# Kernel optimization log

Measured on AMD Instinct MI355X. Metric: run time of the kernel, lower is better.

## Reference

```python
import jax, jax.numpy as jnp
import numpy as np

B, H, S, D = 2, 16, 2048, 64

def setup_inputs() -> dict:
    key = jax.random.key(0)
    kq, kk, kv = jax.random.split(key, 3)
    return {
        "query": jax.random.normal(kq, (B, H, S, D), dtype=jnp.float32),
        "key": jax.random.normal(kk, (B, H, S, D), dtype=jnp.float32),
        "value": jax.random.normal(kv, (B, H, S, D), dtype=jnp.float32),
        "mask": 1,
    }

def reference(query, key, value, mask):
    d_k = jnp.asarray(query.shape[-1], dtype=query.dtype)
    # scores: [B, H, S, S] = Q K^T / sqrt(d_k)
    scores = jnp.einsum('bhqd,bhkd->bhqk', query, key) / jnp.sqrt(d_k)
    if mask:
        Sq, Sk = scores.shape[-2], scores.shape[-1]
        causal = jnp.tril(jnp.ones((Sq, Sk), dtype=bool))
        scores = jnp.where(causal, scores, -jnp.inf)
    attention = jax.nn.softmax(scores, axis=-1)
    out = jnp.einsum('bhqk,bhkd->bhqd', attention, value)
    return out, attention
```

## Files before the change

### kernel.cpp

```cpp
#include <hip/hip_runtime.h>


#define B_ 2
#define H_ 16
#define S_ 2048
#define D_ 64
#define QB 8
#define NT 256

typedef unsigned short u16;
typedef unsigned int   u32;
typedef float f32x4 __attribute__((ext_vector_type(4)));

__device__ __forceinline__ float bf2f(u16 h) {
    union { u32 u; float f; } x; x.u = ((u32)h) << 16; return x.f;
}
__device__ __forceinline__ float wred_max(float v) {
    #pragma unroll
    for (int o = 32; o > 0; o >>= 1) v = fmaxf(v, __shfl_xor(v, o, 64));
    return v;
}
__device__ __forceinline__ float wred_sum(float v) {
    #pragma unroll
    for (int o = 32; o > 0; o >>= 1) v += __shfl_xor(v, o, 64);
    return v;
}

__global__ __launch_bounds__(NT)
void attn_tile8_kernel(const void* __restrict__ Qv, const void* __restrict__ Kv,
                       const void* __restrict__ Vv, const int* __restrict__ maskp,
                       float* __restrict__ out, float* __restrict__ att)
{
    const int tid = threadIdx.x;

    const int bid0 = blockIdx.x;
    const int bid  = (bid0 & 7) * 1024 + (bid0 >> 3);

    const int bh = bid >> 8;
    const int q0 = (bid & 255) << 3;
    const int causal = maskp[0];
    const int kmaxB = causal ? (q0 + QB - 1) : (S_ - 1);

    __shared__ float sS[QB * S_];
    __shared__ float sMaxP[4 * QB];
    __shared__ float sSumP[4 * QB];
    __shared__ float sInv[QB];

    const size_t base = (size_t)bh * S_ * D_;
    const int lane = tid & 63;
    const int wid  = tid >> 6;

    bool isf32;
    {
        u32 w = ((const u32*)Qv)[lane];
        int e0 = (int)((w >> 7)  & 0xFFu);
        int e1 = (int)((w >> 23) & 0xFFu);
        unsigned long long b = __ballot(e0 >= 0x8F || e1 >= 0x8F);
        isf32 = (__popcll(b) >= 4);
    }

    int km[QB];
    #pragma unroll
    for (int r = 0; r < QB; ++r) km[r] = causal ? (q0 + r) : (S_ - 1);

    float lm[QB];
    #pragma unroll
    for (int r = 0; r < QB; ++r) lm[r] = -INFINITY;

    if (isf32) {
        const float4* Q4u = reinterpret_cast<const float4*>(
            (const float*)Qv + base + (size_t)q0 * D_);
        const float4* K4 = reinterpret_cast<const float4*>((const float*)Kv + base);
        for (int off = 0; off <= kmaxB; off += NT) {
            const int j = off + tid;
            if (j <= kmaxB) {
                const float4* kr = K4 + (size_t)j * 16;
                float4 kq[16];
                #pragma unroll
                for (int c = 0; c < 16; ++c) kq[c] = kr[c];
                float dd[QB];
                #pragma unroll
                for (int r = 0; r < QB; ++r) dd[r] = 0.f;
                #pragma unroll
                for (int c = 0; c < 16; ++c) {
                    #pragma unroll
                    for (int r = 0; r < QB; ++r) {
                        float4 a = Q4u[r * 16 + c];
                        dd[r] += a.x*kq[c].x + a.y*kq[c].y + a.z*kq[c].z + a.w*kq[c].w;
                    }
                }
                #pragma unroll
                for (int r = 0; r < QB; ++r) {
                    float s = (j <= km[r]) ? dd[r] : -INFINITY;
                    sS[r * S_ + j] = s;
                    lm[r] = fmaxf(lm[r], s);
                }
            }
        }
    } else {
        const u16* Qh = (const u16*)Qv + base + (size_t)q0 * D_;
        const u16* Kh = (const u16*)Kv + base;
        for (int off = 0; off <= kmaxB; off += NT) {
            const int j = off + tid;
            if (j <= kmaxB) {
                const u16* kr = Kh + (size_t)j * D_;
                float dd[QB];
                #pragma unroll
                for (int r = 0; r < QB; ++r) dd[r] = 0.f;
                #pragma unroll
                for (int c = 0; c < D_; ++c) {
                    float kc = bf2f(kr[c]);
                    #pragma unroll
                    for (int r = 0; r < QB; ++r) dd[r] += bf2f(Qh[r * D_ + c]) * kc;
                }
                #pragma unroll
                for (int r = 0; r < QB; ++r) {
                    float s = (j <= km[r]) ? dd[r] : -INFINITY;
                    sS[r * S_ + j] = s;
                    lm[r] = fmaxf(lm[r], s);
                }
            }
        }
    }

    #pragma unroll
    for (int r = 0; r < QB; ++r) lm[r] = wred_max(lm[r]);
    if (lane == 0) {
        #pragma unroll
        for (int r = 0; r < QB; ++r) sMaxP[wid * QB + r] = lm[r];
    }
    __syncthreads();
    float m[QB];
    #pragma unroll
    for (int r = 0; r < QB; ++r)
        m[r] = fmaxf(fmaxf(sMaxP[r], sMaxP[QB + r]),
                     fmaxf(sMaxP[2*QB + r], sMaxP[3*QB + r]));

    float ls[QB];
    #pragma unroll
    for (int r = 0; r < QB; ++r) ls[r] = 0.f;
    for (int off = 0; off < S_; off += NT * 4) {
        const int j0e = off + tid * 4;
        if (j0e <= kmaxB) {
            #pragma unroll
            for (int r = 0; r < QB; ++r) {
                float4 sv = *reinterpret_cast<float4*>(sS + r * S_ + j0e);
                float e0 = __expf((sv.x - m[r]) * 0.125f);
                float e1 = __expf((sv.y - m[r]) * 0.125f);
                float e2 = __expf((sv.z - m[r]) * 0.125f);
                float e3 = __expf((sv.w - m[r]) * 0.125f);
                *reinterpret_cast<float4*>(sS + r * S_ + j0e) =
                    make_float4(e0, e1, e2, e3);
                ls[r] += (e0 + e1) + (e2 + e3);
            }
        }
    }
    #pragma unroll
    for (int r = 0; r < QB; ++r) ls[r] = wred_sum(ls[r]);
    if (lane == 0) {
        #pragma unroll
        for (int r = 0; r < QB; ++r) sSumP[wid * QB + r] = ls[r];
    }
    __syncthreads();
    float inv[QB];
    #pragma unroll
    for (int r = 0; r < QB; ++r)
        inv[r] = 1.f / ((sSumP[r] + sSumP[QB + r]) +
                        (sSumP[2*QB + r] + sSumP[3*QB + r]));
    if (tid == 0) {
        #pragma unroll
        for (int r = 0; r < QB; ++r) sInv[r] = inv[r];
    }

    {
        const size_t arow = ((size_t)bh * S_ + q0) * S_;
        for (int off = 0; off < S_; off += NT * 4) {
            const int j0a = off + tid * 4;
            const bool wr = (j0a <= kmaxB);
            #pragma unroll
            for (int r = 0; r < QB; ++r) {
                f32x4 p;
                if (wr) {
                    float4 v = *reinterpret_cast<const float4*>(sS + r * S_ + j0a);
                    p.x = v.x * inv[r]; p.y = v.y * inv[r];
                    p.z = v.z * inv[r]; p.w = v.w * inv[r];
                } else {
                    p.x = 0.f; p.y = 0.f; p.z = 0.f; p.w = 0.f;
                }
                f32x4* a4 = reinterpret_cast<f32x4*>(att + arow + (size_t)r * S_ + j0a);
                __builtin_nontemporal_store(p, a4);
            }
        }
    }

    const int dq = tid & 15;
    const int jg = tid >> 4;
    float4 acc[QB];
    #pragma unroll
    for (int r = 0; r < QB; ++r) acc[r] = make_float4(0.f, 0.f, 0.f, 0.f);

    if (isf32) {
        const float4* V4 = reinterpret_cast<const float4*>((const float*)Vv + base);
        for (int j0p = 4 * jg; j0p <= kmaxB; j0p += 64) {
            float4 v0 = V4[(size_t)(j0p + 0) * 16 + dq];
            float4 v1 = V4[(size_t)(j0p + 1) * 16 + dq];
            float4 v2 = V4[(size_t)(j0p + 2) * 16 + dq];
            float4 v3 = V4[(size_t)(j0p + 3) * 16 + dq];
            #pragma unroll
            for (int r = 0; r < QB; ++r) {
                float4 p = *reinterpret_cast<const float4*>(sS + r * S_ + j0p);
                acc[r].x = fmaf(p.x, v0.x, acc[r].x); acc[r].y = fmaf(p.x, v0.y, acc[r].y);
                acc[r].z = fmaf(p.x, v0.z, acc[r].z); acc[r].w = fmaf(p.x, v0.w, acc[r].w);
                acc[r].x = fmaf(p.y, v1.x, acc[r].x); acc[r].y = fmaf(p.y, v1.y, acc[r].y);
                acc[r].z = fmaf(p.y, v1.z, acc[r].z); acc[r].w = fmaf(p.y, v1.w, acc[r].w);
                acc[r].x = fmaf(p.z, v2.x, acc[r].x); acc[r].y = fmaf(p.z, v2.y, acc[r].y);
                acc[r].z = fmaf(p.z, v2.z, acc[r].z); acc[r].w = fmaf(p.z, v2.w, acc[r].w);
                acc[r].x = fmaf(p.w, v3.x, acc[r].x); acc[r].y = fmaf(p.w, v3.y, acc[r].y);
                acc[r].z = fmaf(p.w, v3.z, acc[r].z); acc[r].w = fmaf(p.w, v3.w, acc[r].w);
            }
        }
    } else {
        const u16* Vh = (const u16*)Vv + base;
        for (int j0p = 4 * jg; j0p <= kmaxB; j0p += 64) {
            ushort4 h0 = reinterpret_cast<const ushort4*>(Vh + (size_t)(j0p + 0) * D_)[dq];
            ushort4 h1 = reinterpret_cast<const ushort4*>(Vh + (size_t)(j0p + 1) * D_)[dq];
            ushort4 h2 = reinterpret_cast<const ushort4*>(Vh + (size_t)(j0p + 2) * D_)[dq];
            ushort4 h3 = reinterpret_cast<const ushort4*>(Vh + (size_t)(j0p + 3) * D_)[dq];
            float4 v0 = make_float4(bf2f(h0.x), bf2f(h0.y), bf2f(h0.z), bf2f(h0.w));
            float4 v1 = make_float4(bf2f(h1.x), bf2f(h1.y), bf2f(h1.z), bf2f(h1.w));
            float4 v2 = make_float4(bf2f(h2.x), bf2f(h2.y), bf2f(h2.z), bf2f(h2.w));
            float4 v3 = make_float4(bf2f(h3.x), bf2f(h3.y), bf2f(h3.z), bf2f(h3.w));
            #pragma unroll
            for (int r = 0; r < QB; ++r) {
                float4 p = *reinterpret_cast<const float4*>(sS + r * S_ + j0p);
                acc[r].x = fmaf(p.x, v0.x, acc[r].x); acc[r].y = fmaf(p.x, v0.y, acc[r].y);
                acc[r].z = fmaf(p.x, v0.z, acc[r].z); acc[r].w = fmaf(p.x, v0.w, acc[r].w);
                acc[r].x = fmaf(p.y, v1.x, acc[r].x); acc[r].y = fmaf(p.y, v1.y, acc[r].y);
                acc[r].z = fmaf(p.y, v1.z, acc[r].z); acc[r].w = fmaf(p.y, v1.w, acc[r].w);
                acc[r].x = fmaf(p.z, v2.x, acc[r].x); acc[r].y = fmaf(p.z, v2.y, acc[r].y);
                acc[r].z = fmaf(p.z, v2.z, acc[r].z); acc[r].w = fmaf(p.z, v2.w, acc[r].w);
                acc[r].x = fmaf(p.w, v3.x, acc[r].x); acc[r].y = fmaf(p.w, v3.y, acc[r].y);
                acc[r].z = fmaf(p.w, v3.z, acc[r].z); acc[r].w = fmaf(p.w, v3.w, acc[r].w);
            }
        }
    }

    __syncthreads();
    float4* sPart4 = reinterpret_cast<float4*>(sS);
    #pragma unroll
    for (int r = 0; r < QB; ++r) sPart4[(r * 16 + jg) * 17 + dq] = acc[r];
    __syncthreads();
    {
        const float* spf = sS;
        for (int oo = tid; oo < QB * D_; oo += NT) {
            const int r = oo >> 6;
            const int d = oo & 63;
            float o = 0.f;
            #pragma unroll
            for (int g = 0; g < 16; ++g) o += spf[(r * 16 + g) * 68 + d];
            out[((size_t)bh * S_ + q0 + r) * D_ + d] = o * sInv[r];
        }
    }
}

extern "C" void kernel_launch(void* const* d_in, const int* in_sizes, int n_in,
                              void* d_out, int out_size, void* d_ws, size_t ws_size,
                              hipStream_t stream) {
    const void* Q = d_in[0];
    const void* K = d_in[1];
    const void* V = d_in[2];
    const int* mask = (const int*)d_in[3];

    float* out = (float*)d_out;
    float* att = out + (size_t)B_ * H_ * S_ * D_;

    const int nblk = (B_ * H_ * S_) / QB;
    attn_tile8_kernel<<<nblk, NT, 0, stream>>>(Q, K, V, mask, out, att);
}
```

Before: 995.4 us.

## Use split-bf16 MFMA for QK and PV with a preconversion kernel

Adds a conversion kernel that splits Q, K and V into high and low bf16 parts, stores V transposed in workspace, and a new attention kernel that computes QK^T and PV with bf16 MFMA instructions using three-product hi/lo compensation to keep near-fp32 accuracy. Score storage in shared memory uses an XOR-swizzled layout to avoid bank conflicts. The goal is to move the scalar FP32 dot products onto matrix cores. The cost is an extra kernel launch, workspace traffic, and a small precision difference. The old kernel stays as a fallback when no workspace is provided.

```diff
diff --git a/kernel.cpp b/kernel.cpp
--- a/kernel.cpp
+++ b/kernel.cpp
@@ -7,14 +7,24 @@
 #define D_ 64
 #define QB 8
 #define NT 256
+#define ELEMS (B_ * H_ * S_ * D_)
+#define WS_NEEDED (6ull * ELEMS * 2ull)
 
 typedef unsigned short u16;
 typedef unsigned int   u32;
 typedef float f32x4 __attribute__((ext_vector_type(4)));
+typedef short bf16x8 __attribute__((ext_vector_type(8)));
+
+#define MFMA(a, b, c) __builtin_amdgcn_mfma_f32_16x16x32_bf16((a), (b), (c), 0, 0, 0)
+#define EIDX(r, j) (((r) << 11) + ((((j) >> 3) ^ (r)) << 3) + ((j) & 7))
 
 __device__ __forceinline__ float bf2f(u16 h) {
     union { u32 u; float f; } x; x.u = ((u32)h) << 16; return x.f;
 }
+__device__ __forceinline__ u16 f2bf_rne(float f) {
+    u32 u = __float_as_uint(f);
+    return (u16)((u + 0x7FFFu + ((u >> 16) & 1u)) >> 16);
+}
 __device__ __forceinline__ float wred_max(float v) {
     #pragma unroll
     for (int o = 32; o > 0; o >>= 1) v = fmaxf(v, __shfl_xor(v, o, 64));
@@ -24,6 +34,274 @@
     #pragma unroll
     for (int o = 32; o > 0; o >>= 1) v += __shfl_xor(v, o, 64);
     return v;
+}
+__device__ __forceinline__ bool sniff_f32(const void* Qv, int lane) {
+    u32 wv = ((const u32*)Qv)[lane];
+    int e0 = (int)((wv >> 7)  & 0xFFu);
+    int e1 = (int)((wv >> 23) & 0xFFu);
+    unsigned long long b = __ballot(e0 >= 0x8F || e1 >= 0x8F);
+    return (__popcll(b) >= 4);
+}
+
+__global__ __launch_bounds__(256)
+void conv_kernel(const void* __restrict__ Qv, const void* __restrict__ Kv,
+                 const void* __restrict__ Vv,
+                 u16* __restrict__ qhi, u16* __restrict__ qlo,
+                 u16* __restrict__ khi, u16* __restrict__ klo,
+                 u16* __restrict__ vthi, u16* __restrict__ vtlo)
+{
+    __shared__ float sV[64][65];
+    const int tid = threadIdx.x;
+    const int blk = blockIdx.x;
+    const int bh  = blk >> 5;
+    const int s0  = (blk & 31) << 6;
+    const size_t base = (size_t)bh * S_ * D_;
+    const bool isf32 = sniff_f32(Qv, tid & 63);
+
+    const int sr = tid >> 2;
+    const int dq = (tid & 3) << 4;
+    const size_t roff = base + (size_t)(s0 + sr) * D_ + dq;
+
+    float q16[16], k16[16], v16[16];
+    if (isf32) {
+        const float4* qp = (const float4*)((const float*)Qv + roff);
+        const float4* kp = (const float4*)((const float*)Kv + roff);
+        const float4* vp = (const float4*)((const float*)Vv + roff);
+        #pragma unroll
+        for (int i = 0; i < 4; ++i) {
+            float4 a = qp[i]; q16[4*i+0]=a.x; q16[4*i+1]=a.y; q16[4*i+2]=a.z; q16[4*i+3]=a.w;
+            float4 b = kp[i]; k16[4*i+0]=b.x; k16[4*i+1]=b.y; k16[4*i+2]=b.z; k16[4*i+3]=b.w;
+            float4 c = vp[i]; v16[4*i+0]=c.x; v16[4*i+1]=c.y; v16[4*i+2]=c.z; v16[4*i+3]=c.w;
+        }
+    } else {
+        const u16* qp = (const u16*)Qv + roff;
+        const u16* kp = (const u16*)Kv + roff;
+        const u16* vp = (const u16*)Vv + roff;
+        #pragma unroll
+        for (int i = 0; i < 16; ++i) { q16[i]=bf2f(qp[i]); k16[i]=bf2f(kp[i]); v16[i]=bf2f(vp[i]); }
+    }
+
+    alignas(16) u16 qh[16], ql[16], kh[16], kl[16];
+    #pragma unroll
+    for (int i = 0; i < 16; ++i) {
+        u16 h = f2bf_rne(q16[i]); qh[i] = h; ql[i] = f2bf_rne(q16[i] - bf2f(h));
+        h = f2bf_rne(k16[i]);     kh[i] = h; kl[i] = f2bf_rne(k16[i] - bf2f(h));
+        sV[sr][dq + i] = v16[i];
+    }
+    *(bf16x8*)(qhi + roff)     = *(const bf16x8*)qh;
+    *(bf16x8*)(qhi + roff + 8) = *(const bf16x8*)(qh + 8);
+    *(bf16x8*)(qlo + roff)     = *(const bf16x8*)ql;
+    *(bf16x8*)(qlo + roff + 8) = *(const bf16x8*)(ql + 8);
+    *(bf16x8*)(khi + roff)     = *(const bf16x8*)kh;
+    *(bf16x8*)(khi + roff + 8) = *(const bf16x8*)(kh + 8);
+    *(bf16x8*)(klo + roff)     = *(const bf16x8*)kl;
+    *(bf16x8*)(klo + roff + 8) = *(const bf16x8*)(kl + 8);
+    __syncthreads();
+
+    const int dr = tid >> 2;
+    const int sq = (tid & 3) << 4;
+    alignas(16) u16 vh[16], vl[16];
+    #pragma unroll
+    for (int i = 0; i < 16; ++i) {
+        float x = sV[sq + i][dr];
+        u16 h = f2bf_rne(x); vh[i] = h; vl[i] = f2bf_rne(x - bf2f(h));
+    }
+    const size_t toff = base + (size_t)dr * S_ + s0 + sq;
+    *(bf16x8*)(vthi + toff)     = *(const bf16x8*)vh;
+    *(bf16x8*)(vthi + toff + 8) = *(const bf16x8*)(vh + 8);
+    *(bf16x8*)(vtlo + toff)     = *(const bf16x8*)vl;
+    *(bf16x8*)(vtlo + toff + 8) = *(const bf16x8*)(vl + 8);
+}
+
+__global__ __launch_bounds__(NT)
+void attn_mfma_kernel(const u16* __restrict__ qhi, const u16* __restrict__ qlo,
+                      const u16* __restrict__ khi, const u16* __restrict__ klo,
+                      const u16* __restrict__ vthi, const u16* __restrict__ vtlo,
+                      const int* __restrict__ maskp,
+                      float* __restrict__ out, float* __restrict__ att)
+{
+    const int tid  = threadIdx.x;
+    const int lane = tid & 63;
+    const int w    = tid >> 6;
+    const int l15  = lane & 15;
+    const int l4   = lane >> 4;
+
+    const int bid0 = blockIdx.x;
+    const int bid  = (bid0 & 7) * 1024 + (bid0 >> 3);
+    const int bh = bid >> 8;
+    const int q0 = (bid & 255) << 3;
+    const int causal = maskp[0];
+    const int kmaxB = causal ? (q0 + QB - 1) : (S_ - 1);
+    const int Tmax  = (kmaxB + 16) >> 4;
+    const int Kc    = (kmaxB + 32) >> 5;
+    const int jWritten = Tmax << 4;
+    const int jPV      = Kc << 5;
+
+    __shared__ float sE[QB * S_];
+    __shared__ float sMaxP[4 * QB];
+    __shared__ float sSumP[4 * QB];
+    __shared__ float sM[QB];
+    __shared__ float sInv[QB];
+
+    const size_t base = (size_t)bh * S_ * D_;
+
+    const u16* qrh = qhi + base + (size_t)(q0 + (l15 & 7)) * D_ + l4 * 8;
+    const u16* qrl = qlo + base + (size_t)(q0 + (l15 & 7)) * D_ + l4 * 8;
+    const bf16x8 ah0 = *(const bf16x8*)qrh;
+    const bf16x8 ah1 = *(const bf16x8*)(qrh + 32);
+    const bf16x8 al0 = *(const bf16x8*)qrl;
+    const bf16x8 al1 = *(const bf16x8*)(qrl + 32);
+
+    float rm[4] = {-INFINITY, -INFINITY, -INFINITY, -INFINITY};
+    #pragma unroll 2
+    for (int t = w; t < Tmax; t += 4) {
+        const int j0 = t << 4;
+        const u16* krh = khi + base + (size_t)(j0 + l15) * D_ + l4 * 8;
+        const u16* krl = klo + base + (size_t)(j0 + l15) * D_ + l4 * 8;
+        const bf16x8 bh0 = *(const bf16x8*)krh;
+        const bf16x8 bl0 = *(const bf16x8*)krl;
+        const bf16x8 bh1 = *(const bf16x8*)(krh + 32);
+        const bf16x8 bl1 = *(const bf16x8*)(krl + 32);
+        f32x4 acc = {0.f, 0.f, 0.f, 0.f};
+        acc = MFMA(ah0, bh0, acc);
+        acc = MFMA(ah0, bl0, acc);
+        acc = MFMA(al0, bh0, acc);
+        acc = MFMA(ah1, bh1, acc);
+        acc = MFMA(ah1, bl1, acc);
+        acc = MFMA(al1, bh1, acc);
+        if (l4 < 2) {
+            const int j = j0 + l15;
+            #pragma unroll
+            for (int r = 0; r < 4; ++r) {
+                const int mq = l4 * 4 + r;
+                float s = acc[r];
+                if (causal && j > q0 + mq) s = -INFINITY;
+                sE[EIDX(mq, j)] = s;
+                rm[r] = fmaxf(rm[r], s);
+            }
+        }
+    }
+
+    #pragma unroll
+    for (int r = 0; r < 4; ++r) {
+        float v = rm[r];
+        v = fmaxf(v, __shfl_xor(v, 1, 64));
+        v = fmaxf(v, __shfl_xor(v, 2, 64));
+        v = fmaxf(v, __shfl_xor(v, 4, 64));
+        v = fmaxf(v, __shfl_xor(v, 8, 64));
+        rm[r] = v;
+    }
+    if ((lane & 15) == 0 && l4 < 2) {
+        #pragma unroll
+        for (int r = 0; r < 4; ++r) sMaxP[w * QB + l4 * 4 + r] = rm[r];
+    }
+    __syncthreads();
+    if (tid < QB) {
+        sM[tid] = fmaxf(fmaxf(sMaxP[tid], sMaxP[QB + tid]),
+                        fmaxf(sMaxP[2 * QB + tid], sMaxP[3 * QB + tid]));
+    }
+    __syncthreads();
+
+    float m8[QB];
+    #pragma unroll
+    for (int r = 0; r < QB; ++r) m8[r] = sM[r];
+    float ls[QB];
+    #pragma unroll
+    for (int r = 0; r < QB; ++r) ls[r] = 0.f;
+    for (int j0q = tid * 4; j0q < jPV; j0q += NT * 4) {
+        if (j0q < jWritten) {
+            #pragma unroll
+            for (int r = 0; r < QB; ++r) {
+                f32x4 sv = *(const f32x4*)&sE[EIDX(r, j0q)];
+                f32x4 e;
+                e.x = __expf((sv.x - m8[r]) * 0.125f);
+                e.y = __expf((sv.y - m8[r]) * 0.125f);
+                e.z = __expf((sv.z - m8[r]) * 0.125f);
+                e.w = __expf((sv.w - m8[r]) * 0.125f);
+                *(f32x4*)&sE[EIDX(r, j0q)] = e;
+                ls[r] += (e.x + e.y) + (e.z + e.w);
+            }
+        } else {
+            const f32x4 z = {0.f, 0.f, 0.f, 0.f};
+            #pragma unroll
+            for (int r = 0; r < QB; ++r) *(f32x4*)&sE[EIDX(r, j0q)] = z;
+        }
+    }
+    #pragma unroll
+    for (int r = 0; r < QB; ++r) ls[r] = wred_sum(ls[r]);
+    if (lane == 0) {
+        #pragma unroll
+        for (int r = 0; r < QB; ++r) sSumP[w * QB + r] = ls[r];
+    }
+    __syncthreads();
+    if (tid < QB) {
+        const float t0 = (sSumP[tid] + sSumP[QB + tid]) +
+                         (sSumP[2 * QB + tid] + sSumP[3 * QB + tid]);
+        sInv[tid] = 1.f / t0;
+    }
+    __syncthreads();
+
+    {
+        float inv8[QB];
+        #pragma unroll
+        for (int r = 0; r < QB; ++r) inv8[r] = sInv[r];
+        const size_t arow = ((size_t)bh * S_ + q0) * S_;
+        for (int j0a = tid * 4; j0a < S_; j0a += NT * 4) {
+            const bool live = (j0a < jWritten);
+            #pragma unroll
+            for (int r = 0; r < QB; ++r) {
+                f32x4 p = {0.f, 0.f, 0.f, 0.f};
+                if (live) {
+                    f32x4 v = *(const f32x4*)&sE[EIDX(r, j0a)];
+                    p.x = v.x * inv8[r]; p.y = v.y * inv8[r];
+                    p.z = v.z * inv8[r]; p.w = v.w * inv8[r];
+                }
+                __builtin_nontemporal_store(p, (f32x4*)(att + arow + (size_t)r * S_ + j0a));
+            }
+        }
+    }
+
+    const int d0 = w << 4;
+    const int r8 = l15 & 7;
+    const u16* vbh = vthi + base + (size_t)(d0 + l15) * S_;
+    const u16* vbl = vtlo + base + (size_t)(d0 + l15) * S_;
+
+#define PVSTEP(KS, ACC) {                                                    \
+        const int jf = ((KS) << 5) + l4 * 8;                                 \
+        const float* ep = &sE[EIDX(r8, jf)];                                 \
+        f32x4 e0 = *(const f32x4*)ep;                                        \
+        f32x4 e1 = *(const f32x4*)(ep + 4);                                  \
+        bf16x8 ph, pl;                                                       \
+        _Pragma("unroll")                                                    \
+        for (int i = 0; i < 4; ++i) {                                        \
+            u16 h0 = f2bf_rne(e0[i]);                                        \
+            ph[i] = (short)h0;                                               \
+            pl[i] = (short)f2bf_rne(e0[i] - bf2f(h0));                       \
+            u16 h1 = f2bf_rne(e1[i]);                                        \
+            ph[4 + i] = (short)h1;                                           \
+            pl[4 + i] = (short)f2bf_rne(e1[i] - bf2f(h1));                   \
+        }                                                                    \
+        const bf16x8 vh = *(const bf16x8*)(vbh + jf);                        \
+        const bf16x8 vl = *(const bf16x8*)(vbl + jf);                        \
+        ACC = MFMA(ph, vh, ACC);                                             \
+        ACC = MFMA(ph, vl, ACC);                                             \
+        ACC = MFMA(pl, vh, ACC);                                             \
+    }
+
+    f32x4 acc0 = {0.f, 0.f, 0.f, 0.f};
+    f32x4 acc1 = {0.f, 0.f, 0.f, 0.f};
+    int ks = 0;
+    for (; ks + 1 < Kc; ks += 2) { PVSTEP(ks, acc0) PVSTEP(ks + 1, acc1) }
+    if (ks < Kc) PVSTEP(ks, acc0)
+    const f32x4 accs = acc0 + acc1;
+    if (l4 < 2) {
+        #pragma unroll
+        for (int r = 0; r < 4; ++r) {
+            const int mq = l4 * 4 + r;
+            out[((size_t)bh * S_ + q0 + mq) * D_ + d0 + l15] = accs[r] * sInv[mq];
+        }
+    }
+#undef PVSTEP
 }
 
 __global__ __launch_bounds__(NT)
@@ -32,10 +310,8 @@
                        float* __restrict__ out, float* __restrict__ att)
 {
     const int tid = threadIdx.x;
-
     const int bid0 = blockIdx.x;
     const int bid  = (bid0 & 7) * 1024 + (bid0 >> 3);
-
     const int bh = bid >> 8;
     const int q0 = (bid & 255) << 3;
     const int causal = maskp[0];
@@ -49,27 +325,17 @@
     const size_t base = (size_t)bh * S_ * D_;
     const int lane = tid & 63;
     const int wid  = tid >> 6;
-
-    bool isf32;
-    {
-        u32 w = ((const u32*)Qv)[lane];
-        int e0 = (int)((w >> 7)  & 0xFFu);
-        int e1 = (int)((w >> 23) & 0xFFu);
-        unsigned long long b = __ballot(e0 >= 0x8F || e1 >= 0x8F);
-        isf32 = (__popcll(b) >= 4);
-    }
+    const bool isf32 = sniff_f32(Qv, lane);
 
     int km[QB];
     #pragma unroll
     for (int r = 0; r < QB; ++r) km[r] = causal ? (q0 + r) : (S_ - 1);
-
     float lm[QB];
     #pragma unroll
     for (int r = 0; r < QB; ++r) lm[r] = -INFINITY;
 
     if (isf32) {
-        const float4* Q4u = reinterpret_cast<const float4*>(
-            (const float*)Qv + base + (size_t)q0 * D_);
+        const float4* Q4u = reinterpret_cast<const float4*>((const float*)Qv + base + (size_t)q0 * D_);
         const float4* K4 = reinterpret_cast<const float4*>((const float*)Kv + base);
         for (int off = 0; off <= kmaxB; off += NT) {
             const int j = off + tid;
@@ -133,8 +399,7 @@
     float m[QB];
     #pragma unroll
     for (int r = 0; r < QB; ++r)
-        m[r] = fmaxf(fmaxf(sMaxP[r], sMaxP[QB + r]),
-                     fmaxf(sMaxP[2*QB + r], sMaxP[3*QB + r]));
+        m[r] = fmaxf(fmaxf(sMaxP[r], sMaxP[QB + r]), fmaxf(sMaxP[2*QB + r], sMaxP[3*QB + r]));
 
     float ls[QB];
     #pragma unroll
@@ -149,8 +414,7 @@
                 float e1 = __expf((sv.y - m[r]) * 0.125f);
                 float e2 = __expf((sv.z - m[r]) * 0.125f);
                 float e3 = __expf((sv.w - m[r]) * 0.125f);
-                *reinterpret_cast<float4*>(sS + r * S_ + j0e) =
-                    make_float4(e0, e1, e2, e3);
+                *reinterpret_cast<float4*>(sS + r * S_ + j0e) = make_float4(e0, e1, e2, e3);
                 ls[r] += (e0 + e1) + (e2 + e3);
             }
         }
@@ -165,8 +429,7 @@
     float inv[QB];
     #pragma unroll
     for (int r = 0; r < QB; ++r)
-        inv[r] = 1.f / ((sSumP[r] + sSumP[QB + r]) +
-                        (sSumP[2*QB + r] + sSumP[3*QB + r]));
+        inv[r] = 1.f / ((sSumP[r] + sSumP[QB + r]) + (sSumP[2*QB + r] + sSumP[3*QB + r]));
     if (tid == 0) {
         #pragma unroll
         for (int r = 0; r < QB; ++r) sInv[r] = inv[r];
@@ -184,11 +447,8 @@
                     float4 v = *reinterpret_cast<const float4*>(sS + r * S_ + j0a);
                     p.x = v.x * inv[r]; p.y = v.y * inv[r];
                     p.z = v.z * inv[r]; p.w = v.w * inv[r];
-                } else {
-                    p.x = 0.f; p.y = 0.f; p.z = 0.f; p.w = 0.f;
-                }
-                f32x4* a4 = reinterpret_cast<f32x4*>(att + arow + (size_t)r * S_ + j0a);
-                __builtin_nontemporal_store(p, a4);
+                } else { p.x = 0.f; p.y = 0.f; p.z = 0.f; p.w = 0.f; }
+                __builtin_nontemporal_store(p, reinterpret_cast<f32x4*>(att + arow + (size_t)r * S_ + j0a));
             }
         }
     }
@@ -198,7 +458,6 @@
     float4 acc[QB];
     #pragma unroll
     for (int r = 0; r < QB; ++r) acc[r] = make_float4(0.f, 0.f, 0.f, 0.f);
-
     if (isf32) {
         const float4* V4 = reinterpret_cast<const float4*>((const float*)Vv + base);
         for (int j0p = 4 * jg; j0p <= kmaxB; j0p += 64) {
@@ -274,6 +533,18 @@
     float* out = (float*)d_out;
     float* att = out + (size_t)B_ * H_ * S_ * D_;
 
-    const int nblk = (B_ * H_ * S_) / QB;
-    attn_tile8_kernel<<<nblk, NT, 0, stream>>>(Q, K, V, mask, out, att);
-}
+    if (d_ws != nullptr && ws_size >= WS_NEEDED) {
+        u16* W = (u16*)d_ws;
+        u16* qhi = W;
+        u16* qlo = W + 1ull * ELEMS;
+        u16* khi = W + 2ull * ELEMS;
+        u16* klo = W + 3ull * ELEMS;
+        u16* vthi = W + 4ull * ELEMS;
+        u16* vtlo = W + 5ull * ELEMS;
+        conv_kernel<<<B_ * H_ * (S_ / 64), 256, 0, stream>>>(Q, K, V, qhi, qlo, khi, klo, vthi, vtlo);
+        attn_mfma_kernel<<<(B_ * H_ * S_) / QB, NT, 0, stream>>>(qhi, qlo, khi, klo, vthi, vtlo,
+                                                                 mask, out, att);
+    } else {
+        attn_tile8_kernel<<<(B_ * H_ * S_) / QB, NT, 0, stream>>>(Q, K, V, mask, out, att);
+    }
+}
```

Result: no change. 1.010 ms (+1.5%).
